# Optimization experiments

Measured on AMD Instinct MI355X. Metric: run time of the kernel, lower is better.

The kernel has to match this reference:

```python
import jax, jax.numpy as jnp
import numpy as np

P, L, H = 3, 4, 6          # window size, num scales, num heads
EPS = 1e-5                 # LayerNorm eps (PyTorch default)


def setup_inputs() -> dict:
    key = jax.random.key(0)
    B, T, D = 8, 4096, 768
    ks = jax.random.split(key, 12)
    s = 0.02
    w = lambda k, shape: (jax.random.normal(k, shape, jnp.float32) * s)
    z = lambda n: jnp.zeros((n,), jnp.float32)
    return {
        "x": jax.random.normal(ks[0], (B, T, D), jnp.float32),
        "ln_g": jnp.ones((D,), jnp.float32),
        "ln_b": z(D),
        "qw": w(ks[1], (D, D)), "qb": z(D),
        "kw": w(ks[2], (D, D)), "kb": z(D),
        "vw": w(ks[3], (D, D)), "vb": z(D),
        "inw": w(ks[4], (3 * D, D)), "inb": z(3 * D),   # MHA in_proj
        "mow": w(ks[5], (D, D)), "mob": z(D),            # MHA out_proj
        "ow": w(ks[6], (D, D)), "ob": z(D),              # output_proj
    }


def _layernorm(x, g, b):
    mu = jnp.mean(x, -1, keepdims=True)
    var = jnp.mean((x - mu) ** 2, -1, keepdims=True)
    return (x - mu) * jax.lax.rsqrt(var + EPS) * g + b


def _mha_windows(q, k, v, inw, inb, mow, mob):
    # q,k,v: [B, W, P, D] -- batched tiny attention over all windows at once
    B, W, Pw, D = q.shape
    hd = D // H
    wq, wk, wv = inw[:D], inw[D:2 * D], inw[2 * D:]
    bq, bk, bv = inb[:D], inb[D:2 * D], inb[2 * D:]
    qp = (q @ wq.T + bq).reshape(B, W, Pw, H, hd)
    kp = (k @ wk.T + bk).reshape(B, W, Pw, H, hd)
    vp = (v @ wv.T + bv).reshape(B, W, Pw, H, hd)
    scores = jnp.einsum('bwqhd,bwkhd->bwhqk', qp, kp) / jnp.sqrt(jnp.float32(hd))
    attn = jax.nn.softmax(scores, axis=-1)
    o = jnp.einsum('bwhqk,bwkhd->bwqhd', attn, vp).reshape(B, W, Pw, D)
    return o @ mow.T + mob


def reference(x, ln_g, ln_b, qw, qb, kw, kb, vw, vb, inw, inb, mow, mob, ow, ob):
    B, T, D = x.shape
    xn = _layernorm(x, ln_g, ln_b)
    Q = xn @ qw.T + qb
    K = xn @ kw.T + kb
    V = xn @ vw.T + vb
    acc = jnp.zeros_like(x)
    for kk in range(L):
        scale = P ** kk
        if T < scale:
            continue
        Lp = T // scale
        pool = lambda z: z[:, :Lp * scale].reshape(B, Lp, scale, D).mean(axis=2)
        pQ, pK, pV = pool(Q), pool(K), pool(V)
        W = Lp // P
        if W == 0:
            continue
        win = lambda z: z[:, :W * P].reshape(B, W, P, D)
        o = _mha_windows(win(pQ), win(pK), win(pV), inw, inb, mow, mob)
        so = o.reshape(B, W * P, D)                       # concat of windows
        idx = (jnp.arange(T) * (W * P)) // T              # nearest interp to T
        up = so[:, idx]
        acc = acc + jax.nn.gelu(up, approximate=False)    # exact GELU (torch default)
    out = acc @ ow.T + ob
    return x + out
```

## Files before the change

kernel.cpp:

```cpp
#include <hip/hip_runtime.h>
#include <stdint.h>

typedef short s16x8 __attribute__((ext_vector_type(8)));
typedef float f32x4 __attribute__((ext_vector_type(4)));

__device__ __forceinline__ unsigned short f2bf(float f) {
  unsigned u = __builtin_bit_cast(unsigned, f);
  u = (u + 0x7FFFu + ((u >> 16) & 1u)) >> 16;
  return (unsigned short)u;
}
__device__ __forceinline__ float bf2f(unsigned short h) {
  unsigned u = ((unsigned)h) << 16;
  return __builtin_bit_cast(float, u);
}

__device__ __forceinline__ void gload_lds16(const void* g, void* l) {
  __builtin_amdgcn_global_load_lds((__attribute__((address_space(1))) void*)g,
                                   (__attribute__((address_space(3))) void*)l,
                                   16, 0, 0);
}

__global__ __launch_bounds__(256)
void mstr_convw(const float* __restrict__ inw, const float* __restrict__ mow,
                const float* __restrict__ ow, unsigned short* __restrict__ inwB,
                unsigned short* __restrict__ mowB, unsigned short* __restrict__ owB)
{
  long i = (long)blockIdx.x * 256 + threadIdx.x;
  const long n1 = 589824;
  if (i < 3 * n1)      inwB[i] = f2bf(inw[i]);
  else if (i < 4 * n1) mowB[i - 3 * n1] = f2bf(mow[i - 3 * n1]);
  else                 owB[i - 4 * n1] = f2bf(ow[i - 4 * n1]);
}

__global__ __launch_bounds__(256)
void mstr_transpose(const float* __restrict__ qw, const float* __restrict__ kw,
                    const float* __restrict__ vw, unsigned short* __restrict__ wT)
{
  const float* src = (blockIdx.z == 0) ? qw : (blockIdx.z == 1) ? kw : vw;
  unsigned short* dst = wT + (long)blockIdx.z * 589824;
  __shared__ float tile[32][33];
  int tx = threadIdx.x & 31, ty = threadIdx.x >> 5;
  int j0 = blockIdx.x * 32, k0 = blockIdx.y * 32;
#pragma unroll
  for (int i = 0; i < 4; ++i)
    tile[ty + i * 8][tx] = src[(long)(j0 + ty + i * 8) * 768 + k0 + tx];
  __syncthreads();
#pragma unroll
  for (int i = 0; i < 4; ++i)
    dst[(long)(k0 + ty + i * 8) * 768 + j0 + tx] = f2bf(tile[tx][ty + i * 8]);
}

__global__ __launch_bounds__(256)
void mstr_biascomb(const float* __restrict__ inw, const float* __restrict__ inb,
                   const float* __restrict__ qb, const float* __restrict__ kb,
                   const float* __restrict__ vb, float* __restrict__ bc,
                   float* __restrict__ zb)
{
  int gid = blockIdx.x * 256 + threadIdx.x;
  if (gid < 768) zb[gid] = 0.f;
  int s = gid / 768, c = gid - s * 768;
  const float* b = (s == 0) ? qb : (s == 1) ? kb : vb;
  const float* wrow = inw + (long)(s * 768 + c) * 768;
  float a = inb[s * 768 + c];
  for (int j = 0; j < 768; ++j) a += b[j] * wrow[j];
  bc[gid] = a;
}

__global__ __launch_bounds__(256)
void mstr_ln(const float* __restrict__ x, const float* __restrict__ g,
             const float* __restrict__ bt, unsigned short* __restrict__ xn)
{
  int blk = blockIdx.x;
  int bb = blk / 4095, t = blk - bb * 4095;
  const float* xr = x + ((long)bb * 4096 + t) * 768;
  unsigned short* orow = xn + (long)blk * 768;
  int tid = threadIdx.x;
  float v0 = xr[tid], v1 = xr[tid + 256], v2 = xr[tid + 512];
  float s = v0 + v1 + v2;
  float s2 = v0 * v0 + v1 * v1 + v2 * v2;
#pragma unroll
  for (int o = 32; o > 0; o >>= 1) { s += __shfl_down(s, o, 64); s2 += __shfl_down(s2, o, 64); }
  __shared__ float rs[4], rq[4];
  int lane = tid & 63, wid = tid >> 6;
  if (lane == 0) { rs[wid] = s; rq[wid] = s2; }
  __syncthreads();
  float S = rs[0] + rs[1] + rs[2] + rs[3];
  float S2 = rq[0] + rq[1] + rq[2] + rq[3];
  float mu = S * (1.0f / 768.0f);
  float var = S2 * (1.0f / 768.0f) - mu * mu;
  float rstd = rsqrtf(var + 1e-5f);
  orow[tid] = f2bf((v0 - mu) * rstd * g[tid] + bt[tid]);
  orow[tid + 256] = f2bf((v1 - mu) * rstd * g[tid + 256] + bt[tid + 256]);
  orow[tid + 512] = f2bf((v2 - mu) * rstd * g[tid + 512] + bt[tid + 512]);
}

template<int EPI>
__global__ __launch_bounds__(256)
void mstr_gemm(const unsigned short* __restrict__ A, int M,
               const unsigned short* __restrict__ W,
               const float* __restrict__ bias,
               unsigned short* __restrict__ out0,
               unsigned short* __restrict__ out1,
               unsigned short* __restrict__ out2,
               float* __restrict__ outf,
               const float* __restrict__ xadd,
               int rowDiv, int rowStride, int NC, int nwg)
{
  int orig = blockIdx.x;
  int swq = nwg >> 3, swr = nwg & 7;
  int xcd = orig & 7, sidx = orig >> 3;
  int wg = (xcd < swr ? xcd * (swq + 1) : swr * (swq + 1) + (xcd - swr) * swq) + sidx;
  int rowp = wg / NC, colp = wg - rowp * NC;

  __shared__ unsigned short As[128 * 32];
  __shared__ unsigned short Bs[128 * 32];
  const int tid = threadIdx.x;
  const int lane = tid & 63;
  const int wid = tid >> 6;
  const int wr = wid >> 1, wc = wid & 1;
  const long row0 = (long)rowp * 128;
  const int col0 = colp * 128;
  const unsigned short* Bg = W + (long)col0 * 768;
  const int sr = tid >> 2;
  const int sc = (tid & 3) * 8;
  const int fr = lane & 15;
  const int fk = (lane >> 4) * 8;
  long rA0 = row0 + sr;       if (rA0 >= M) rA0 = M - 1;
  long rA1 = row0 + sr + 64;  if (rA1 >= M) rA1 = M - 1;
  const unsigned short* AgR0 = A + rA0 * 768 + sc;
  const unsigned short* AgR1 = A + rA1 * 768 + sc;
  const unsigned short* BgR0 = Bg + (long)sr * 768 + sc;
  const unsigned short* BgR1 = Bg + (long)(sr + 64) * 768 + sc;
  f32x4 acc[4][4] = {};
  for (int k0 = 0; k0 < 768; k0 += 32) {
    __syncthreads();
    gload_lds16(AgR0 + k0, (char*)As + tid * 16);
    gload_lds16(AgR1 + k0, (char*)As + 4096 + tid * 16);
    gload_lds16(BgR0 + k0, (char*)Bs + tid * 16);
    gload_lds16(BgR1 + k0, (char*)Bs + 4096 + tid * 16);
    __syncthreads();
    s16x8 af[4], bfv[4];
#pragma unroll
    for (int m = 0; m < 4; ++m)
      af[m] = *(const s16x8*)(&As[(wr * 64 + m * 16 + fr) * 32 + fk]);
#pragma unroll
    for (int n = 0; n < 4; ++n)
      bfv[n] = *(const s16x8*)(&Bs[(wc * 64 + n * 16 + fr) * 32 + fk]);
#pragma unroll
    for (int m = 0; m < 4; ++m)
#pragma unroll
      for (int n = 0; n < 4; ++n)
        acc[m][n] = __builtin_amdgcn_mfma_f32_16x16x32_bf16(af[m], bfv[n], acc[m][n], 0, 0, 0);
  }
  int seg = (col0 >= 1536) ? 2 : (col0 >= 768 ? 1 : 0);
  unsigned short* outp = (seg == 0) ? out0 : (seg == 1) ? out1 : out2;
  int csub = seg * 768;
#pragma unroll
  for (int m = 0; m < 4; ++m) {
#pragma unroll
    for (int r = 0; r < 4; ++r) {
      long gr = row0 + wr * 64 + m * 16 + (lane >> 4) * 4 + r;
      if (gr < M) {
        long orow;
        if (EPI == 0) {
          int qq = (int)gr / rowDiv;
          orow = (long)qq * rowStride + ((int)gr - qq * rowDiv);
        } else {
          orow = gr;
        }
#pragma unroll
        for (int n = 0; n < 4; ++n) {
          int c = col0 + wc * 64 + n * 16 + (lane & 15);
          float v = acc[m][n][r] + bias[c];
          if (EPI == 0) {
            outp[orow * 768 + (c - csub)] = f2bf(v);
          } else {
            long o = orow * 768 + c;
            outf[o] = v + xadd[o];
          }
        }
      }
    }
  }
}

__global__ __launch_bounds__(384)
void mstr_pool(unsigned short* qp, unsigned short* kp, unsigned short* vp,
               int srcOff, int dstOff, int Ndst)
{
  unsigned short* p = (blockIdx.y == 0) ? qp : (blockIdx.y == 1) ? kp : vp;
  int tok = blockIdx.x;
  int bb = tok / Ndst, j = tok - bb * Ndst;
  long sb = ((long)bb * 6063 + srcOff + 3 * j) * 768 + threadIdx.x * 2;
  long db = ((long)bb * 6063 + dstOff + j) * 768 + threadIdx.x * 2;
  unsigned a = *(const unsigned*)(p + sb);
  unsigned b = *(const unsigned*)(p + sb + 768);
  unsigned c = *(const unsigned*)(p + sb + 1536);
  float lo = (bf2f((unsigned short)a) + bf2f((unsigned short)b) + bf2f((unsigned short)c)) * (1.0f / 3.0f);
  float hi = (bf2f((unsigned short)(a >> 16)) + bf2f((unsigned short)(b >> 16)) + bf2f((unsigned short)(c >> 16))) * (1.0f / 3.0f);
  unsigned o = (unsigned)f2bf(lo) | ((unsigned)f2bf(hi) << 16);
  *(unsigned*)(p + db) = o;
}

__global__ __launch_bounds__(256)
void mstr_attn(unsigned short* qp, unsigned short* kp, unsigned short* vp, int nwaves)
{
  int gw = blockIdx.x * 4 + (threadIdx.x >> 6);
  if (gw >= nwaves) return;
  int lane = threadIdx.x & 63;
  int win = gw / 6, h = gw - win * 6;
  int bb = win / 2021, ww = win - bb * 2021;
  int row0;
  if (ww < 1365)      row0 = 3 * ww;
  else if (ww < 1820) row0 = 4095 + 3 * (ww - 1365);
  else if (ww < 1971) row0 = 5460 + 3 * (ww - 1820);
  else                row0 = 5913 + 3 * (ww - 1971);
  long base = ((long)bb * 6063 + row0) * 768 + h * 128 + lane * 2;
  float q[3][2], k[3][2], v[3][2];
#pragma unroll
  for (int i = 0; i < 3; ++i) {
    unsigned uq = *(const unsigned*)(qp + base + i * 768);
    unsigned uk = *(const unsigned*)(kp + base + i * 768);
    unsigned uv = *(const unsigned*)(vp + base + i * 768);
    q[i][0] = bf2f((unsigned short)uq); q[i][1] = bf2f((unsigned short)(uq >> 16));
    k[i][0] = bf2f((unsigned short)uk); k[i][1] = bf2f((unsigned short)(uk >> 16));
    v[i][0] = bf2f((unsigned short)uv); v[i][1] = bf2f((unsigned short)(uv >> 16));
  }
  float s[3][3];
#pragma unroll
  for (int i = 0; i < 3; ++i)
#pragma unroll
    for (int j = 0; j < 3; ++j)
      s[i][j] = q[i][0] * k[j][0] + q[i][1] * k[j][1];
#pragma unroll
  for (int st = 1; st < 64; st <<= 1) {
#pragma unroll
    for (int i = 0; i < 3; ++i)
#pragma unroll
      for (int j = 0; j < 3; ++j)
        s[i][j] += __shfl_xor(s[i][j], st, 64);
  }
  const float scl = 0.088388347648318447f;
#pragma unroll
  for (int i = 0; i < 3; ++i) {
    float s0 = s[i][0] * scl, s1 = s[i][1] * scl, s2 = s[i][2] * scl;
    float m = fmaxf(s0, fmaxf(s1, s2));
    float e0 = __expf(s0 - m), e1 = __expf(s1 - m), e2 = __expf(s2 - m);
    float inv = 1.0f / (e0 + e1 + e2);
    e0 *= inv; e1 *= inv; e2 *= inv;
    float o0 = e0 * v[0][0] + e1 * v[1][0] + e2 * v[2][0];
    float o1 = e0 * v[0][1] + e1 * v[1][1] + e2 * v[2][1];
    unsigned o = (unsigned)f2bf(o0) | ((unsigned)f2bf(o1) << 16);
    *(unsigned*)(qp + base + i * 768) = o;
  }
}

__global__ __launch_bounds__(256)
void mstr_gelusum(const unsigned short* __restrict__ omo, unsigned short* __restrict__ acc)
{
  long gid = (long)blockIdx.x * 256 + threadIdx.x;
  int d2 = (int)(gid % 384);
  long row = gid / 384;
  int bb = (int)(row >> 12);
  int t = (int)(row & 4095);
  const int NkA[4] = {4095, 1365, 453, 150};
  const int soA[4] = {0, 4095, 5460, 5913};
  float a0 = 0.f, a1 = 0.f;
#pragma unroll
  for (int kk = 0; kk < 4; ++kk) {
    int idx = (t * NkA[kk]) >> 12;
    long tok = (long)bb * 6063 + soA[kk] + idx;
    unsigned u = *(const unsigned*)(omo + tok * 768 + d2 * 2);
    float x0 = bf2f((unsigned short)u), x1 = bf2f((unsigned short)(u >> 16));
    a0 += 0.5f * x0 * (1.0f + erff(x0 * 0.70710678118654752f));
    a1 += 0.5f * x1 * (1.0f + erff(x1 * 0.70710678118654752f));
  }
  unsigned o = (unsigned)f2bf(a0) | ((unsigned)f2bf(a1) << 16);
  *(unsigned*)(acc + row * 768 + d2 * 2) = o;
}

extern "C" void kernel_launch(void* const* d_in, const int* in_sizes, int n_in,
                              void* d_out, int out_size, void* d_ws, size_t ws_size,
                              hipStream_t stream)
{
  const float* x   = (const float*)d_in[0];
  const float* lng = (const float*)d_in[1];
  const float* lnb = (const float*)d_in[2];
  const float* qw  = (const float*)d_in[3];
  const float* qb  = (const float*)d_in[4];
  const float* kw  = (const float*)d_in[5];
  const float* kb  = (const float*)d_in[6];
  const float* vw  = (const float*)d_in[7];
  const float* vb  = (const float*)d_in[8];
  const float* inw = (const float*)d_in[9];
  const float* inb = (const float*)d_in[10];
  const float* mob = (const float*)d_in[12];
  const float* ow  = (const float*)d_in[13];
  const float* ob  = (const float*)d_in[14];

  const long n1 = 589824;
  char* ws = (char*)d_ws;
  size_t off = 0;
  auto alloc = [&](size_t bytes) -> char* {
    char* p = ws + off;
    off += (bytes + 255) & ~(size_t)255;
    return p;
  };
  unsigned short* Wc = (unsigned short*)alloc((size_t)5 * n1 * 2);
  float* bc = (float*)alloc(2304 * 4);
  float* zb = (float*)alloc(768 * 4);
  size_t fixed = off;

  int g = 0;
  const int cands[4] = {8, 4, 2, 1};
  for (int ci = 0; ci < 4; ++ci) {
    int c = cands[ci];
    size_t need = fixed + (size_t)c * 4096 * 768 * 2
                + 2 * (size_t)c * 6063 * 768 * 2
                + 1024;
    if (need <= ws_size) { g = c; break; }
  }
  if (!g) return;

  char* GR = ws + fixed;
  unsigned short* xnacc = (unsigned short*)GR;
  unsigned short* qp = xnacc + (size_t)g * 4096 * 768;
  unsigned short* kp = qp + (size_t)g * 6063 * 768;
  unsigned short* inwB = (unsigned short*)GR;
  unsigned short* wT   = inwB + 3 * n1;

  unsigned short* mowB = Wc + 3 * n1;
  unsigned short* owB  = Wc + 4 * n1;

  mstr_convw<<<dim3(11520), dim3(256), 0, stream>>>(inw, (const float*)d_in[11], ow, inwB, mowB, owB);
  mstr_transpose<<<dim3(24, 24, 3), dim3(256), 0, stream>>>(qw, kw, vw, wT);
  mstr_biascomb<<<dim3(9), dim3(256), 0, stream>>>(inw, inb, qb, kb, vb, bc, zb);
  for (int s = 0; s < 3; ++s)
    mstr_gemm<0><<<dim3(36), dim3(256), 0, stream>>>(inwB + (long)s * n1, 768, wT + (long)s * n1,
                                                     zb, Wc + (long)s * n1, Wc + (long)s * n1,
                                                     Wc + (long)s * n1, nullptr, nullptr, 768, 768, 6, 36);

  int ng = 8 / g;
  for (int gi = 0; gi < ng; ++gi) {
    const float* xg = x + (long)gi * g * 4096 * 768;
    unsigned short* vp = (unsigned short*)d_out + (long)gi * g * 4096 * 768 * 2;
    mstr_ln<<<dim3(g * 4095), dim3(256), 0, stream>>>(xg, lng, lnb, xnacc);
    int M1 = g * 4095, gb1 = (M1 + 127) / 128;
    int nwg1 = gb1 * 18;
    mstr_gemm<0><<<dim3(nwg1), dim3(256), 0, stream>>>(xnacc, M1, Wc, bc,
                                                       qp, kp, vp, nullptr, nullptr,
                                                       4095, 6063, 18, nwg1);
    mstr_pool<<<dim3(g * 1365, 3), dim3(384), 0, stream>>>(qp, kp, vp, 0, 4095, 1365);
    mstr_pool<<<dim3(g * 453, 3), dim3(384), 0, stream>>>(qp, kp, vp, 4095, 5460, 453);
    mstr_pool<<<dim3(g * 150, 3), dim3(384), 0, stream>>>(qp, kp, vp, 5460, 5913, 150);
    int nw = g * 2021 * 6;
    mstr_attn<<<dim3((nw + 3) / 4), dim3(256), 0, stream>>>(qp, kp, vp, nw);
    int M2 = g * 6063;
    int nwg2 = ((M2 + 127) / 128) * 6;
    mstr_gemm<0><<<dim3(nwg2), dim3(256), 0, stream>>>(qp, M2, mowB, mob, kp, kp, kp,
                                                       nullptr, nullptr, M2, 0, 6, nwg2);
    mstr_gelusum<<<dim3(g * 6144), dim3(256), 0, stream>>>(kp, xnacc);
    int M3 = g * 4096;
    int nwg3 = (M3 / 128) * 6;
    mstr_gemm<1><<<dim3(nwg3), dim3(256), 0, stream>>>(xnacc, M3, owB, ob, nullptr, nullptr, nullptr,
                                                       (float*)d_out + (long)gi * g * 4096 * 768, xg,
                                                       M3, 0, 6, nwg3);
  }
}
```

Before: 628.1 us.

## Pipeline GEMM K-loop with 4-stage swizzled LDS ring and fuse GELU into out-proj

New measurement: 641.9 us. 1.02x slower.

```diff
diff --git a/kernel.cpp b/kernel.cpp
--- a/kernel.cpp
+++ b/kernel.cpp
@@ -95,63 +95,80 @@
 }
 
 template<int EPI>
-__global__ __launch_bounds__(256)
+__global__ __launch_bounds__(256, 2)
 void mstr_gemm(const unsigned short* __restrict__ A, int M,
                const unsigned short* __restrict__ W,
                const float* __restrict__ bias,
-               unsigned short* __restrict__ out0,
-               unsigned short* __restrict__ out1,
-               unsigned short* __restrict__ out2,
-               float* __restrict__ outf,
-               const float* __restrict__ xadd,
+               unsigned short* out0, unsigned short* out1, unsigned short* out2,
+               float* outf, const float* xadd,
                int rowDiv, int rowStride, int NC, int nwg)
 {
+  __shared__ char smem[65536];
   int orig = blockIdx.x;
   int swq = nwg >> 3, swr = nwg & 7;
   int xcd = orig & 7, sidx = orig >> 3;
   int wg = (xcd < swr ? xcd * (swq + 1) : swr * (swq + 1) + (xcd - swr) * swq) + sidx;
   int rowp = wg / NC, colp = wg - rowp * NC;
 
-  __shared__ unsigned short As[128 * 32];
-  __shared__ unsigned short Bs[128 * 32];
   const int tid = threadIdx.x;
   const int lane = tid & 63;
   const int wid = tid >> 6;
   const int wr = wid >> 1, wc = wid & 1;
   const long row0 = (long)rowp * 128;
   const int col0 = colp * 128;
-  const unsigned short* Bg = W + (long)col0 * 768;
+
   const int sr = tid >> 2;
-  const int sc = (tid & 3) * 8;
+  const int sc = (((tid & 3) ^ ((tid >> 3) & 3)) << 3);
+  long a0r = row0 + sr;       if (a0r >= M) a0r = M - 1;
+  long a1r = row0 + sr + 64;  if (a1r >= M) a1r = M - 1;
+  const unsigned short* Ag0 = A + a0r * 768 + sc;
+  const unsigned short* Ag1 = A + a1r * 768 + sc;
+  const unsigned short* Bg0 = W + (long)(col0 + sr) * 768 + sc;
+  const unsigned short* Bg1 = W + (long)(col0 + sr + 64) * 768 + sc;
+  char* ldsT = smem + tid * 16;
+
   const int fr = lane & 15;
-  const int fk = (lane >> 4) * 8;
-  long rA0 = row0 + sr;       if (rA0 >= M) rA0 = M - 1;
-  long rA1 = row0 + sr + 64;  if (rA1 >= M) rA1 = M - 1;
-  const unsigned short* AgR0 = A + rA0 * 768 + sc;
-  const unsigned short* AgR1 = A + rA1 * 768 + sc;
-  const unsigned short* BgR0 = Bg + (long)sr * 768 + sc;
-  const unsigned short* BgR1 = Bg + (long)(sr + 64) * 768 + sc;
+  const int g4 = lane >> 4;
+  const int cx = ((g4 ^ ((fr >> 1) & 3)) << 4);
+  const int aoff = (wr * 64 + fr) * 64 + cx;
+  const int boff = 8192 + (wc * 64 + fr) * 64 + cx;
+
   f32x4 acc[4][4] = {};
-  for (int k0 = 0; k0 < 768; k0 += 32) {
-    __syncthreads();
-    gload_lds16(AgR0 + k0, (char*)As + tid * 16);
-    gload_lds16(AgR1 + k0, (char*)As + 4096 + tid * 16);
-    gload_lds16(BgR0 + k0, (char*)Bs + tid * 16);
-    gload_lds16(BgR1 + k0, (char*)Bs + 4096 + tid * 16);
-    __syncthreads();
+
+#define MSTAGE(T) { int kk_ = (T) * 32; int bo_ = ((T) & 3) * 16384; \
+    gload_lds16(Ag0 + kk_, ldsT + bo_); \
+    gload_lds16(Ag1 + kk_, ldsT + bo_ + 4096); \
+    gload_lds16(Bg0 + kk_, ldsT + bo_ + 8192); \
+    gload_lds16(Bg1 + kk_, ldsT + bo_ + 12288); }
+
+  MSTAGE(0) MSTAGE(1) MSTAGE(2)
+  asm volatile("s_waitcnt vmcnt(8)" ::: "memory");
+  __builtin_amdgcn_s_barrier();
+
+  for (int t = 0; t < 24; ++t) {
+    if (t < 21) MSTAGE(t + 3)
+    const int bo = (t & 3) * 16384;
     s16x8 af[4], bfv[4];
 #pragma unroll
-    for (int m = 0; m < 4; ++m)
-      af[m] = *(const s16x8*)(&As[(wr * 64 + m * 16 + fr) * 32 + fk]);
-#pragma unroll
-    for (int n = 0; n < 4; ++n)
-      bfv[n] = *(const s16x8*)(&Bs[(wc * 64 + n * 16 + fr) * 32 + fk]);
+    for (int m = 0; m < 4; ++m) af[m] = *(const s16x8*)(smem + bo + aoff + m * 1024);
+#pragma unroll
+    for (int n = 0; n < 4; ++n) bfv[n] = *(const s16x8*)(smem + bo + boff + n * 1024);
+    __builtin_amdgcn_s_setprio(1);
 #pragma unroll
     for (int m = 0; m < 4; ++m)
 #pragma unroll
       for (int n = 0; n < 4; ++n)
         acc[m][n] = __builtin_amdgcn_mfma_f32_16x16x32_bf16(af[m], bfv[n], acc[m][n], 0, 0, 0);
-  }
+    __builtin_amdgcn_s_setprio(0);
+    if (t < 23) {
+      if (t < 21)       asm volatile("s_waitcnt vmcnt(8)" ::: "memory");
+      else if (t == 21) asm volatile("s_waitcnt vmcnt(4)" ::: "memory");
+      else              asm volatile("s_waitcnt vmcnt(0)" ::: "memory");
+      __builtin_amdgcn_s_barrier();
+    }
+  }
+#undef MSTAGE
+
   int seg = (col0 >= 1536) ? 2 : (col0 >= 768 ? 1 : 0);
   unsigned short* outp = (seg == 0) ? out0 : (seg == 1) ? out1 : out2;
   int csub = seg * 768;
@@ -159,24 +176,27 @@
   for (int m = 0; m < 4; ++m) {
 #pragma unroll
     for (int r = 0; r < 4; ++r) {
-      long gr = row0 + wr * 64 + m * 16 + (lane >> 4) * 4 + r;
+      long gr = row0 + wr * 64 + m * 16 + g4 * 4 + r;
       if (gr < M) {
         long orow;
-        if (EPI == 0) {
+        if (EPI == 1) {
+          orow = gr;
+        } else {
           int qq = (int)gr / rowDiv;
           orow = (long)qq * rowStride + ((int)gr - qq * rowDiv);
-        } else {
-          orow = gr;
         }
 #pragma unroll
         for (int n = 0; n < 4; ++n) {
-          int c = col0 + wc * 64 + n * 16 + (lane & 15);
+          int c = col0 + wc * 64 + n * 16 + fr;
           float v = acc[m][n][r] + bias[c];
-          if (EPI == 0) {
+          if (EPI == 1) {
+            long o = gr * 768 + c;
+            outf[o] = v + xadd[o];
+          } else if (EPI == 2) {
+            v = 0.5f * v * (1.0f + erff(v * 0.70710678118654752f));
             outp[orow * 768 + (c - csub)] = f2bf(v);
           } else {
-            long o = orow * 768 + c;
-            outf[o] = v + xadd[o];
+            outp[orow * 768 + (c - csub)] = f2bf(v);
           }
         }
       }
@@ -271,9 +291,8 @@
     int idx = (t * NkA[kk]) >> 12;
     long tok = (long)bb * 6063 + soA[kk] + idx;
     unsigned u = *(const unsigned*)(omo + tok * 768 + d2 * 2);
-    float x0 = bf2f((unsigned short)u), x1 = bf2f((unsigned short)(u >> 16));
-    a0 += 0.5f * x0 * (1.0f + erff(x0 * 0.70710678118654752f));
-    a1 += 0.5f * x1 * (1.0f + erff(x1 * 0.70710678118654752f));
+    a0 += bf2f((unsigned short)u);
+    a1 += bf2f((unsigned short)(u >> 16));
   }
   unsigned o = (unsigned)f2bf(a0) | ((unsigned)f2bf(a1) << 16);
   *(unsigned*)(acc + row * 768 + d2 * 2) = o;
@@ -357,7 +376,7 @@
     mstr_attn<<<dim3((nw + 3) / 4), dim3(256), 0, stream>>>(qp, kp, vp, nw);
     int M2 = g * 6063;
     int nwg2 = ((M2 + 127) / 128) * 6;
-    mstr_gemm<0><<<dim3(nwg2), dim3(256), 0, stream>>>(qp, M2, mowB, mob, kp, kp, kp,
+    mstr_gemm<2><<<dim3(nwg2), dim3(256), 0, stream>>>(qp, M2, mowB, mob, kp, kp, kp,
                                                        nullptr, nullptr, M2, 0, 6, nwg2);
     mstr_gelusum<<<dim3(g * 6144), dim3(256), 0, stream>>>(kp, xnacc);
     int M3 = g * 4096;
```
